# Optimization experiments

Hardware: AMD Instinct MI355X
Metric: run time of the kernel (lower is better)

Reference implementation:

```python
import itertools
import jax, jax.numpy as jnp
import numpy as np

KERNEL = (2, 2)
NIN = 4            # prod(KERNEL)
NPAT = 16          # 2 ** NIN
# Faithful to the torch code: every kernel offset shifts dim 0 (the transposes
# swap dims 1 and d+1 and never touch dim 0), so each flattened kernel slot is a
# roll of x along axis 0 by -(sum of offsets), row-major over kernel indices.
SHIFTS = tuple(sum(idx) for idx in itertools.product(*(range(k) for k in KERNEL)))
BITS = np.asarray(list(itertools.product((0, 1), repeat=NIN)), dtype=np.float32)  # (NPAT, NIN)


def setup_inputs() -> dict:
    key = jax.random.key(0)
    k1, k2 = jax.random.split(key)
    x = jax.random.uniform(k1, (256, 64, 64), dtype=jnp.float32)                 # inputs in [0,1)
    toggle_gates = jax.random.uniform(k2, (4, NPAT, 64, 64), dtype=jnp.float32)  # torch.rand init
    return {"x": x, "toggle_gates": toggle_gates}


def _convolve(v):
    # (B,H,W) -> (B,H,W,NIN): shifted neighbor stack (rolls along dim 0, as in the torch code)
    return jnp.stack([jnp.roll(v, -s, axis=0) for s in SHIFTS], axis=-1)


def _pattern_weights(conv):
    # weight[b,h,w,p] = prod_j (conv_j if bit_j(p) else 1-conv_j)
    # equals prod_j (1 - |bit_j(p) - conv_j|) since bits are 0/1
    bits = jnp.asarray(BITS)  # (NPAT, NIN)
    w = jnp.ones(conv.shape[:-1] + (NPAT,), conv.dtype)
    for j in range(NIN):  # NIN=4, small fixed loop
        vj = conv[..., j:j + 1]  # (B,H,W,1)
        w = w * (vj * bits[:, j] + (1.0 - vj) * (1.0 - bits[:, j]))
    return w  # (B,H,W,NPAT)


def reference(x, toggle_gates):
    layers = toggle_gates.shape[0]
    tw = jax.nn.sigmoid(toggle_gates)  # (L,NPAT,H,W)
    outputs = x
    reg = jnp.asarray(0.0, x.dtype)
    for i in range(layers):
        conv = _convolve(outputs)          # (B,H,W,NIN)
        w = _pattern_weights(conv)         # (B,H,W,NPAT)
        if i:
            reg = reg - (jnp.mean(jnp.log(w)) + jnp.mean(jnp.log(1.0 - w)))
        # (weight * toggle).sum over pattern axis
        outputs = jnp.clip(jnp.einsum('bhwp,phw->bhw', w, tw[i]), 0.0, 1.0)
    return outputs, reg / (layers - 1)
```

## Files before the change

### kernel.cpp

```cpp
#include <hip/hip_runtime.h>

#define BATCH 256
#define HWSZ  4096
#define COLS  16
#define BSTR  17

__global__ __launch_bounds__(256) void fused_kernel(
    const float* __restrict__ x,
    const float* __restrict__ tg,
    float* __restrict__ out,
    float* __restrict__ partials)
{
    __shared__ float bufA[BATCH * BSTR];
    __shared__ float bufB[BATCH * BSTR];
    __shared__ float tws[64 * COLS];
    __shared__ float wsum[4];

    const int tid  = threadIdx.x;
    const int hw0  = blockIdx.x * COLS;
    const int c    = tid & 15;
    const int brow = tid >> 4;
    const int b0   = brow * 16;

#pragma unroll
    for (int k = 0; k < 4; ++k) {
        int idx = tid + k * 256;
        int c2 = idx & 15;
        int lp = idx >> 4;
        float g = tg[lp * HWSZ + hw0 + c2];
        tws[lp * COLS + c2] = 1.0f / (1.0f + __expf(-g));
    }

#pragma unroll
    for (int k = 0; k < 16; ++k) {
        int idx = tid + k * 256;
        int b = idx >> 4;
        int c2 = idx & 15;
        bufA[b * BSTR + c2] = x[b * HWSZ + hw0 + c2];
    }

    float racc = 0.0f;
    float* src = bufA;
    float* dst = bufB;

#pragma unroll
    for (int l = 0; l < 4; ++l) {
        __syncthreads();

        const float* tl = &tws[l * 16 * COLS + c];
        float T0  = tl[0 * COLS], T1 = tl[1 * COLS];
        float T24 = tl[2 * COLS] + tl[4 * COLS];
        float T35 = tl[3 * COLS] + tl[5 * COLS];
        float T6  = tl[6 * COLS], T7 = tl[7 * COLS];
        float T8  = tl[8 * COLS], T9 = tl[9 * COLS];
        float TAC = tl[10 * COLS] + tl[12 * COLS];
        float TBD = tl[11 * COLS] + tl[13 * COLS];
        float TE  = tl[14 * COLS], TF = tl[15 * COLS];

        float v0 = src[b0 * BSTR + c];
        float v1 = src[(b0 + 1) * BSTR + c];

#pragma unroll
        for (int k = 0; k < 16; ++k) {
            float v2 = src[((b0 + k + 2) & 255) * BSTR + c];
            float a0 = 1.0f - v0, a1 = 1.0f - v1, a2 = 1.0f - v2;

            float g0 = a1 * a1, g1 = a1 * v1, g2 = v1 * v1;
            float u00 = a0 * g0, u01 = a0 * g1, u02 = a0 * g2;
            float u10 = v0 * g0, u11 = v0 * g1, u12 = v0 * g2;

            float w0 = u00 * a2, w1 = u00 * v2;
            float w2 = u01 * a2, w3 = u01 * v2;
            float w6 = u02 * a2, w7 = u02 * v2;
            float w8 = u10 * a2, w9 = u10 * v2;
            float wA = u11 * a2, wB = u11 * v2;
            float wE = u12 * a2, wF = u12 * v2;

            float acc = w0 * T0 + w1 * T1 + w2 * T24 + w3 * T35
                      + w6 * T6 + w7 * T7 + w8 * T8 + w9 * T9
                      + wA * TAC + wB * TBD + wE * TE + wF * TF;
            float o = fminf(fmaxf(acc, 0.0f), 1.0f);

            if (l == 3) out[(b0 + k) * HWSZ + hw0 + c] = o;
            else        dst[(b0 + k) * BSTR + c] = o;

            if (l >= 1) {
                float s1 = (1.0f - w0) * (1.0f - w1) * (1.0f - w6) * (1.0f - w7)
                         * (1.0f - w8) * (1.0f - w9) * (1.0f - wE) * (1.0f - wF);
                float s2 = (1.0f - w2) * (1.0f - w3) * (1.0f - wA) * (1.0f - wB);
                float pB = s1 * s2 * s2;
                float pA = (v0 * a0) * (g1 * g1) * (v2 * a2);
                racc += 8.0f * __logf(pA) + __logf(pB);
            }
            v0 = v1; v1 = v2;
        }
        float* t = src; src = dst; dst = t;
    }

#pragma unroll
    for (int off = 32; off; off >>= 1) racc += __shfl_down(racc, off, 64);
    if ((tid & 63) == 0) wsum[tid >> 6] = racc;
    __syncthreads();
    if (tid == 0) partials[blockIdx.x] = wsum[0] + wsum[1] + wsum[2] + wsum[3];
}

__global__ void finalize_kernel(const float* __restrict__ partials,
                                float* __restrict__ out_reg)
{
    int tid = threadIdx.x;
    double v = (double)partials[tid];
#pragma unroll
    for (int off = 32; off; off >>= 1) v += __shfl_down(v, off, 64);
    __shared__ double ws[4];
    if ((tid & 63) == 0) ws[tid >> 6] = v;
    __syncthreads();
    if (tid == 0) {
        double tot = ws[0] + ws[1] + ws[2] + ws[3];
        out_reg[0] = (float)(-tot / (16777216.0 * 3.0));
    }
}

extern "C" void kernel_launch(void* const* d_in, const int* in_sizes, int n_in,
                              void* d_out, int out_size, void* d_ws, size_t ws_size,
                              hipStream_t stream)
{
    const float* x  = (const float*)d_in[0];
    const float* tg = (const float*)d_in[1];
    float* out      = (float*)d_out;
    float* partials = (float*)d_ws;

    fused_kernel<<<dim3(HWSZ / COLS), dim3(256), 0, stream>>>(x, tg, out, partials);
    finalize_kernel<<<1, 256, 0, stream>>>(partials, out + (size_t)BATCH * HWSZ);
}
```

Baseline: 72.10 us.

## Shrink column tile to 4 for more blocks and fuse finalize via last-block atomic

Cuts the column tile from 16 to 4, raising the grid from 256 to 1024 blocks so each thread handles 4 batch rows instead of 16 and the GPU's CUs fill better. The separate finalize kernel is dropped: each block writes its partial sum and bumps an atomic counter, and the last block reduces all partials. This removes a kernel launch but adds a memset launch. Narrow 4-float columns make the global loads and stores less coalesced (16-byte segments per row), and each block recomputes halo reads more often.

```diff
diff --git a/kernel.cpp b/kernel.cpp
--- a/kernel.cpp
+++ b/kernel.cpp
@@ -2,40 +2,39 @@
 
 #define BATCH 256
 #define HWSZ  4096
-#define COLS  16
-#define BSTR  17
+#define COLS  4
+#define BSTR  5
+#define NBLK  (HWSZ / COLS)
 
 __global__ __launch_bounds__(256) void fused_kernel(
     const float* __restrict__ x,
     const float* __restrict__ tg,
     float* __restrict__ out,
-    float* __restrict__ partials)
+    float* __restrict__ partials,
+    unsigned int* __restrict__ counter,
+    float* __restrict__ out_reg)
 {
     __shared__ float bufA[BATCH * BSTR];
     __shared__ float bufB[BATCH * BSTR];
     __shared__ float tws[64 * COLS];
     __shared__ float wsum[4];
+    __shared__ int lastflag;
 
     const int tid  = threadIdx.x;
     const int hw0  = blockIdx.x * COLS;
-    const int c    = tid & 15;
-    const int brow = tid >> 4;
-    const int b0   = brow * 16;
+    const int c    = tid & (COLS - 1);
+    const int brow = tid >> 2;
+    const int b0   = brow * 4;
 
+    {
+        int c2 = tid & 3, lp = tid >> 2;
+        float g = tg[lp * HWSZ + hw0 + c2];
+        tws[lp * COLS + c2] = 1.0f / (1.0f + __expf(-g));
+    }
 #pragma unroll
     for (int k = 0; k < 4; ++k) {
         int idx = tid + k * 256;
-        int c2 = idx & 15;
-        int lp = idx >> 4;
-        float g = tg[lp * HWSZ + hw0 + c2];
-        tws[lp * COLS + c2] = 1.0f / (1.0f + __expf(-g));
-    }
-
-#pragma unroll
-    for (int k = 0; k < 16; ++k) {
-        int idx = tid + k * 256;
-        int b = idx >> 4;
-        int c2 = idx & 15;
+        int b = idx >> 2, c2 = idx & 3;
         bufA[b * BSTR + c2] = x[b * HWSZ + hw0 + c2];
     }
 
@@ -61,7 +60,7 @@
         float v1 = src[(b0 + 1) * BSTR + c];
 
 #pragma unroll
-        for (int k = 0; k < 16; ++k) {
+        for (int k = 0; k < 4; ++k) {
             float v2 = src[((b0 + k + 2) & 255) * BSTR + c];
             float a0 = 1.0f - v0, a1 = 1.0f - v1, a2 = 1.0f - v2;
 
@@ -101,22 +100,29 @@
     for (int off = 32; off; off >>= 1) racc += __shfl_down(racc, off, 64);
     if ((tid & 63) == 0) wsum[tid >> 6] = racc;
     __syncthreads();
-    if (tid == 0) partials[blockIdx.x] = wsum[0] + wsum[1] + wsum[2] + wsum[3];
-}
 
-__global__ void finalize_kernel(const float* __restrict__ partials,
-                                float* __restrict__ out_reg)
-{
-    int tid = threadIdx.x;
-    double v = (double)partials[tid];
+    if (tid == 0) {
+        partials[blockIdx.x] = wsum[0] + wsum[1] + wsum[2] + wsum[3];
+        __threadfence();
+        unsigned int t = atomicAdd(counter, 1u);
+        lastflag = (t == NBLK - 1);
+    }
+    __syncthreads();
+
+    if (lastflag) {
+        __threadfence();
+        double v = 0.0;
 #pragma unroll
-    for (int off = 32; off; off >>= 1) v += __shfl_down(v, off, 64);
-    __shared__ double ws[4];
-    if ((tid & 63) == 0) ws[tid >> 6] = v;
-    __syncthreads();
-    if (tid == 0) {
-        double tot = ws[0] + ws[1] + ws[2] + ws[3];
-        out_reg[0] = (float)(-tot / (16777216.0 * 3.0));
+        for (int i = 0; i < NBLK / 256; ++i) v += (double)partials[tid + i * 256];
+#pragma unroll
+        for (int off = 32; off; off >>= 1) v += __shfl_down(v, off, 64);
+        __shared__ double dsum[4];
+        if ((tid & 63) == 0) dsum[tid >> 6] = v;
+        __syncthreads();
+        if (tid == 0) {
+            double tot = dsum[0] + dsum[1] + dsum[2] + dsum[3];
+            out_reg[0] = (float)(-tot / (16777216.0 * 3.0));
+        }
     }
 }
 
@@ -128,7 +134,9 @@
     const float* tg = (const float*)d_in[1];
     float* out      = (float*)d_out;
     float* partials = (float*)d_ws;
+    unsigned int* counter = (unsigned int*)((char*)d_ws + NBLK * sizeof(float));
 
-    fused_kernel<<<dim3(HWSZ / COLS), dim3(256), 0, stream>>>(x, tg, out, partials);
-    finalize_kernel<<<1, 256, 0, stream>>>(partials, out + (size_t)BATCH * HWSZ);
+    hipMemsetAsync(counter, 0, sizeof(unsigned int), stream);
+    fused_kernel<<<dim3(NBLK), dim3(256), 0, stream>>>(
+        x, tg, out, partials, counter, out + (size_t)BATCH * HWSZ);
 }
```

After: 107.0 us. 1.48x slower.
